# Performance work log

Hardware: AMD Instinct MI355X
Metric: run time of the kernel (lower is better)

## Reference

```python
import jax, jax.numpy as jnp
import numpy as np

N = 100000
E = 1600000
D_IN = 128
HID = 128
N_CLASSES = 40
NEG_SLOPE = 0.2  # PyG GATConv default
BN_EPS = 1e-5


def setup_inputs() -> dict:
    key = jax.random.key(0)
    ks = jax.random.split(key, 16)
    s = 0.1
    return {
        "x": jax.random.normal(ks[0], (N, D_IN), dtype=jnp.float32),
        "edge_index": jax.random.randint(ks[1], (2, E), 0, N, dtype=jnp.int64),
        # GAT layer 1 (in=D_IN, out=HID, heads=1)
        "W1": jax.random.normal(ks[2], (D_IN, HID), dtype=jnp.float32) * s,
        "a_src1": jax.random.normal(ks[3], (HID,), dtype=jnp.float32) * s,
        "a_dst1": jax.random.normal(ks[4], (HID,), dtype=jnp.float32) * s,
        "b1": jnp.zeros((HID,), dtype=jnp.float32),
        # GAT layer 2 (in=HID, out=HID, heads=1)
        "W2": jax.random.normal(ks[5], (HID, HID), dtype=jnp.float32) * s,
        "a_src2": jax.random.normal(ks[6], (HID,), dtype=jnp.float32) * s,
        "a_dst2": jax.random.normal(ks[7], (HID,), dtype=jnp.float32) * s,
        "b2": jnp.zeros((HID,), dtype=jnp.float32),
        # shared BatchNorm1d(HID) applied after every conv
        "gamma": jnp.ones((HID,), dtype=jnp.float32),
        "beta": jnp.zeros((HID,), dtype=jnp.float32),
        # output Linear(HID, N_CLASSES)
        "Wout": jax.random.normal(ks[8], (HID, N_CLASSES), dtype=jnp.float32) * s,
        "bout": jnp.zeros((N_CLASSES,), dtype=jnp.float32),
    }


def reference(x, edge_index, W1, a_src1, a_dst1, b1, W2, a_src2, a_dst2, b2,
              gamma, beta, Wout, bout):
    n = x.shape[0]
    loops = jnp.arange(n, dtype=edge_index.dtype)  # add_self_loops (GATConv default)
    src = jnp.concatenate([edge_index[0], loops])
    dst = jnp.concatenate([edge_index[1], loops])

    def gat_layer(h_in, W, a_s, a_d, b):
        h = h_in @ W                                   # [N, HID]
        e_src = h @ a_s                                # [N] per-node src score
        e_dst = h @ a_d                                # [N] per-node dst score
        e = jax.nn.leaky_relu(e_src[src] + e_dst[dst], NEG_SLOPE)  # [E+N]
        # segment softmax over incoming edges of each dst node
        m = jax.ops.segment_max(e, dst, num_segments=n)
        p = jnp.exp(e - m[dst])
        denom = jax.ops.segment_sum(p, dst, num_segments=n)
        alpha = p / denom[dst]
        out = jax.ops.segment_sum(alpha[:, None] * h[src], dst, num_segments=n)
        return out + b

    def bn_elu(z):
        mu = z.mean(axis=0)
        var = ((z - mu) ** 2).mean(axis=0)  # biased var (BN training mode)
        zh = (z - mu) / jnp.sqrt(var + BN_EPS) * gamma + beta
        return jax.nn.elu(zh)

    h = bn_elu(gat_layer(x, W1, a_src1, a_dst1, b1))
    h = bn_elu(gat_layer(h, W2, a_src2, a_dst2, b2))
    return h @ Wout + bout
```

## Files before the change

kernel.cpp:

```cpp
#include <hip/hip_runtime.h>

#define NNODES 100000
#define NEDGES 1600000
#define ET (NEDGES + NNODES)
#define NBUCK 196
#define NEG 0.2f
#define BNEPS 1e-5f
#define EPB 16384
#define NBLK_E ((ET + EPB - 1) / EPB)

typedef __attribute__((ext_vector_type(8))) short short8;
typedef __attribute__((ext_vector_type(4))) float floatx4;
typedef __attribute__((ext_vector_type(2))) float floatx2;

__device__ __forceinline__ unsigned short f2b(float x) {
    unsigned int u = __float_as_uint(x);
    u += 0x7fff + ((u >> 16) & 1);
    return (unsigned short)(u >> 16);
}
__device__ __forceinline__ float b2f(unsigned short u) {
    return __uint_as_float(((unsigned int)u) << 16);
}
__device__ __forceinline__ float blo2f(unsigned int v) {
    return __uint_as_float(v << 16);
}
__device__ __forceinline__ float bhi2f(unsigned int v) {
    return __uint_as_float(v & 0xffff0000u);
}
__device__ __forceinline__ floatx2 u2f2(unsigned int v) {
    floatx2 r;
    r.x = __uint_as_float(v << 16);
    r.y = __uint_as_float(v & 0xffff0000u);
    return r;
}

__device__ __forceinline__ int edge_src(const int* ei, int e, int w64) {
    if (e >= NEDGES) return e - NEDGES;
    return w64 ? ei[2 * e] : ei[e];
}
__device__ __forceinline__ int edge_dst(const int* ei, int e, int w64) {
    if (e >= NEDGES) return e - NEDGES;
    return w64 ? ei[2 * (NEDGES + e)] : ei[NEDGES + e];
}

__global__ void k_prep(const float* __restrict__ W1, const float* __restrict__ W2,
                       unsigned short* __restrict__ WT1, unsigned short* __restrict__ WT2,
                       const int* ei, int* flag, int* bcnt, int* done, float* bnstat) {
    int t = blockIdx.x * 256 + threadIdx.x;
    if (blockIdx.x == 0) {
        bcnt[threadIdx.x] = 0;
        if (threadIdx.x == 0) *done = 0;
        if (threadIdx.x == 1) {
            int is64 = 1;
            for (int j = 1; j < 16; j += 2)
                if (ei[j] != 0) is64 = 0;
            *flag = is64;
        }
    } else if (blockIdx.x == 1) {
        bnstat[threadIdx.x] = 0.f;
    } else if (blockIdx.x == 2) {
        bnstat[256 + threadIdx.x] = 0.f;
    }
    int k = t >> 7, n = t & 127;
    WT1[n * 128 + k] = f2b(W1[t]);
    WT2[n * 128 + k] = f2b(W2[t]);
}

__global__ __launch_bounds__(256) void k_bhist(const int* __restrict__ ei,
                                               const int* flag, int* bcnt,
                                               int* done, int* bbase, int* bcur) {
    __shared__ int lc[256];
    __shared__ int lastf;
    int t = threadIdx.x;
    lc[t] = 0;
    __syncthreads();
    int w64 = *flag;
    int base = blockIdx.x * EPB;
    for (int j = 0; j < EPB / 512; j++) {
        int e = base + j * 512 + t * 2;
        if (e + 1 < NEDGES) {
            int d0, d1;
            if (w64) {
                int4 dv = *(const int4*)&ei[2 * (NEDGES + e)];
                d0 = dv.x; d1 = dv.z;
            } else {
                int2 dv = *(const int2*)&ei[NEDGES + e];
                d0 = dv.x; d1 = dv.y;
            }
            atomicAdd(&lc[d0 >> 9], 1);
            atomicAdd(&lc[d1 >> 9], 1);
        } else {
            for (int k = 0; k < 2; k++) {
                int ee = e + k;
                if (ee < ET) atomicAdd(&lc[edge_dst(ei, ee, w64) >> 9], 1);
            }
        }
    }
    __syncthreads();
    if (t < NBUCK && lc[t]) atomicAdd(&bcnt[t], lc[t]);
    __threadfence();
    __syncthreads();
    if (t == 0) lastf = (atomicAdd(done, 1) == gridDim.x - 1) ? 1 : 0;
    __syncthreads();
    if (!lastf) return;
    int v = (t < NBUCK) ? atomicAdd(&bcnt[t], 0) : 0;
    __syncthreads();
    lc[t] = v;
    __syncthreads();
    for (int off = 1; off < 256; off <<= 1) {
        int add = (t >= off) ? lc[t - off] : 0;
        __syncthreads();
        lc[t] += add;
        __syncthreads();
    }
    int excl = lc[t] - v;
    if (t < NBUCK) { bbase[t] = excl; bcur[t] = excl; }
    if (t == NBUCK - 1) bbase[NBUCK] = excl + v;
}

__global__ __launch_bounds__(256) void k_bscatter(const int* __restrict__ ei,
                                                  const int* flag, int* bcur,
                                                  int* __restrict__ pairs) {
    __shared__ int lc[256];
    __shared__ int lbase[256];
    int t = threadIdx.x;
    lc[t] = 0;
    __syncthreads();
    int w64 = *flag;
    int base = blockIdx.x * EPB;
    for (int j = 0; j < EPB / 512; j++) {
        int e = base + j * 512 + t * 2;
        if (e + 1 < NEDGES) {
            int d0, d1;
            if (w64) {
                int4 dv = *(const int4*)&ei[2 * (NEDGES + e)];
                d0 = dv.x; d1 = dv.z;
            } else {
                int2 dv = *(const int2*)&ei[NEDGES + e];
                d0 = dv.x; d1 = dv.y;
            }
            atomicAdd(&lc[d0 >> 9], 1);
            atomicAdd(&lc[d1 >> 9], 1);
        } else {
            for (int k = 0; k < 2; k++) {
                int ee = e + k;
                if (ee < ET) atomicAdd(&lc[edge_dst(ei, ee, w64) >> 9], 1);
            }
        }
    }
    __syncthreads();
    if (t < NBUCK && lc[t]) lbase[t] = atomicAdd(&bcur[t], lc[t]);
    __syncthreads();
    for (int j = 0; j < EPB / 512; j++) {
        int e = base + j * 512 + t * 2;
        if (e + 1 < NEDGES) {
            int s0, s1, d0, d1;
            if (w64) {
                int4 sv = *(const int4*)&ei[2 * e];
                int4 dv = *(const int4*)&ei[2 * (NEDGES + e)];
                s0 = sv.x; s1 = sv.z; d0 = dv.x; d1 = dv.z;
            } else {
                int2 sv = *(const int2*)&ei[e];
                int2 dv = *(const int2*)&ei[NEDGES + e];
                s0 = sv.x; s1 = sv.y; d0 = dv.x; d1 = dv.y;
            }
            int p0 = atomicAdd(&lbase[d0 >> 9], 1);
            pairs[p0] = (s0 << 9) | (d0 & 511);
            int p1 = atomicAdd(&lbase[d1 >> 9], 1);
            pairs[p1] = (s1 << 9) | (d1 & 511);
        } else {
            for (int k = 0; k < 2; k++) {
                int ee = e + k;
                if (ee < ET) {
                    int src = edge_src(ei, ee, w64);
                    int dst = edge_dst(ei, ee, w64);
                    int pos = atomicAdd(&lbase[dst >> 9], 1);
                    pairs[pos] = (src << 9) | (dst & 511);
                }
            }
        }
    }
}

__global__ __launch_bounds__(256) void k_bsort(const int* __restrict__ pairs,
                                               const int* __restrict__ bbase,
                                               int* __restrict__ rowptr,
                                               int* __restrict__ srcs) {
    __shared__ int ncnt[512];
    __shared__ int nbase[512];
    __shared__ int stmp[256];
    int b = blockIdx.x, t = threadIdx.x;
    ncnt[t] = 0; ncnt[t + 256] = 0;
    __syncthreads();
    int s0 = bbase[b], s1 = bbase[b + 1];
    for (int i = s0 + t; i < s1; i += 256)
        atomicAdd(&ncnt[pairs[i] & 511], 1);
    __syncthreads();
    int c0 = ncnt[2 * t], c1 = ncnt[2 * t + 1];
    int s = c0 + c1;
    stmp[t] = s;
    __syncthreads();
    for (int off = 1; off < 256; off <<= 1) {
        int add = (t >= off) ? stmp[t - off] : 0;
        __syncthreads();
        stmp[t] += add;
        __syncthreads();
    }
    int excl = stmp[t] - s;
    nbase[2 * t] = excl;
    nbase[2 * t + 1] = excl + c0;
    __syncthreads();
    for (int l = t; l < 512; l += 256) {
        int node = b * 512 + l;
        if (node <= NNODES) rowptr[node] = s0 + nbase[l];
        ncnt[l] = nbase[l];
    }
    __syncthreads();
    for (int i = s0 + t; i < s1; i += 256) {
        int pr = pairs[i];
        int off = atomicAdd(&ncnt[pr & 511], 1);
        srcs[s0 + off] = ((unsigned int)pr) >> 9;
    }
}

template<bool BN>
__global__ __launch_bounds__(256) void k_gemm(const void* __restrict__ Ain,
        const unsigned short* __restrict__ WTg,
        const float* __restrict__ sums, const float* __restrict__ sqs,
        const float* __restrict__ gamma, const float* __restrict__ beta,
        const float* __restrict__ a_s, const float* __restrict__ a_d,
        float* __restrict__ es, float* __restrict__ ed,
        unsigned short* __restrict__ hB, int n) {
    __shared__ unsigned short lA[64][136];
    __shared__ unsigned short lW[128][136];
    __shared__ float las[128], lad[128];
    __shared__ float lsc[128], lsh[128];
    int t = threadIdx.x;
    int row0 = blockIdx.x * 64;
    if (t < 128) { las[t] = a_s[t]; lad[t] = a_d[t]; }
    if (BN && t < 128) {
        float mu = sums[t] * (1.f / NNODES);
        float var = fmaxf(sqs[t] * (1.f / NNODES) - mu * mu, 0.f);
        float s = gamma[t] * rsqrtf(var + BNEPS);
        lsc[t] = s;
        lsh[t] = beta[t] - mu * s;
    }

    const uint4* wt4 = (const uint4*)WTg;
#pragma unroll
    for (int j = 0; j < 8; j++) {
        int idx = t + j * 256;
        *(uint4*)&lW[idx >> 4][(idx & 15) * 8] = wt4[idx];
    }
    if (BN) __syncthreads();

    if (BN) {
        const uint4* Ab = (const uint4*)Ain;
#pragma unroll
        for (int j = 0; j < 4; j++) {
            int idx = t + j * 256;
            int r = idx >> 4, seg = idx & 15;
            uint4 v = make_uint4(0, 0, 0, 0);
            if (row0 + r < n) v = Ab[(size_t)(row0 + r) * 16 + seg];
            float f[8];
            f[0] = blo2f(v.x); f[1] = bhi2f(v.x);
            f[2] = blo2f(v.y); f[3] = bhi2f(v.y);
            f[4] = blo2f(v.z); f[5] = bhi2f(v.z);
            f[6] = blo2f(v.w); f[7] = bhi2f(v.w);
            ushort4 u0, u1;
            unsigned short us[8];
#pragma unroll
            for (int k = 0; k < 8; k++) {
                int c = seg * 8 + k;
                float z = fmaf(f[k], lsc[c], lsh[c]);
                z = z > 0.f ? z : __expf(z) - 1.f;
                us[k] = f2b(z);
            }
            u0.x = us[0]; u0.y = us[1]; u0.z = us[2]; u0.w = us[3];
            u1.x = us[4]; u1.y = us[5]; u1.z = us[6]; u1.w = us[7];
            *(ushort4*)&lA[r][seg * 8] = u0;
            *(ushort4*)&lA[r][seg * 8 + 4] = u1;
        }
    } else {
        const float* Af = (const float*)Ain;
#pragma unroll
        for (int j = 0; j < 8; j++) {
            int idx = t + j * 256;
            int r = idx >> 5, c4 = idx & 31;
            float4 v = make_float4(0.f, 0.f, 0.f, 0.f);
            if (row0 + r < n) v = ((const float4*)Af)[(size_t)(row0 + r) * 32 + c4];
            ushort4 u;
            u.x = f2b(v.x); u.y = f2b(v.y); u.z = f2b(v.z); u.w = f2b(v.w);
            *(ushort4*)&lA[r][c4 * 4] = u;
        }
    }
    __syncthreads();

    int w = t >> 6, lane = t & 63;
    int m = lane & 15, q = lane >> 4;
    int arow = w * 16 + m;
    floatx4 acc[8];
#pragma unroll
    for (int ct = 0; ct < 8; ct++) acc[ct] = (floatx4)0.0f;

#pragma unroll
    for (int kt = 0; kt < 4; kt++) {
        int kb = kt * 32 + q * 8;
        short8 af = *(const short8*)&lA[arow][kb];
#pragma unroll
        for (int ct = 0; ct < 8; ct++) {
            short8 bf = *(const short8*)&lW[ct * 16 + m][kb];
            acc[ct] = __builtin_amdgcn_mfma_f32_16x16x32_bf16(af, bf, acc[ct], 0, 0, 0);
        }
    }

    __syncthreads();
#pragma unroll
    for (int ct = 0; ct < 8; ct++)
#pragma unroll
        for (int r = 0; r < 4; r++)
            lA[w * 16 + q * 4 + r][ct * 16 + m] = f2b(acc[ct][r]);
#pragma unroll
    for (int j = 0; j < 4; j++) {
        int idx = lane + j * 64;
        int r = idx >> 4, seg = idx & 15;
        int grow = row0 + w * 16 + r;
        if (grow < n) {
            uint4 v = *(const uint4*)&lA[w * 16 + r][seg * 8];
            ((uint4*)hB)[(size_t)grow * 16 + seg] = v;
        }
    }
    __syncthreads();
    int r = t >> 2, q4 = t & 3;
    float s1 = 0.f, s2 = 0.f;
#pragma unroll
    for (int k = 0; k < 32; k++) {
        int c = q4 * 32 + k;
        float v = b2f(lA[r][c]);
        s1 += v * las[c];
        s2 += v * lad[c];
    }
    s1 += __shfl_xor(s1, 1, 64); s1 += __shfl_xor(s1, 2, 64);
    s2 += __shfl_xor(s2, 1, 64); s2 += __shfl_xor(s2, 2, 64);
    if (q4 == 0 && row0 + r < n) { es[row0 + r] = s1; ed[row0 + r] = s2; }
}

__global__ __launch_bounds__(256) void k_attn(const unsigned short* __restrict__ hB,
                                              const int* __restrict__ srcs,
                                              const int* __restrict__ rowptr,
                                              const float* __restrict__ es,
                                              const float* __restrict__ ed,
                                              const float* __restrict__ bias,
                                              unsigned short* __restrict__ haggB, int n) {
    int w = (blockIdx.x * 256 + threadIdx.x) >> 4;
    if (w >= n) return;
    int l = threadIdx.x & 15;
    int qb = threadIdx.x & 48;
    int start = rowptr[w], end = rowptr[w + 1];
    float edv = ed[w];
    const uint4* hp4 = (const uint4*)hB;
    floatx2 a0 = {0.f, 0.f}, a1 = {0.f, 0.f}, a2 = {0.f, 0.f}, a3 = {0.f, 0.f};
    float den = 0.f;

    for (int chunk = start; chunk < end; chunk += 16) {
        int i = chunk + l;
        int sv = 0; float pv = 0.f;
        if (i < end) {
            sv = srcs[i];
            float e = es[sv] + edv;
            e = e > 0.f ? e : NEG * e;
            pv = __expf(e);
            den += pv;
        }
        int cnt = min(16, end - chunk);
        for (int j = 0; j < cnt; j++) {
            int   s0 = __shfl(sv, qb + j, 64);
            float p0 = __shfl(pv, qb + j, 64);
            uint4 h0 = hp4[(size_t)s0 * 16 + l];
            floatx2 P = {p0, p0};
            a0 += P * u2f2(h0.x); a1 += P * u2f2(h0.y);
            a2 += P * u2f2(h0.z); a3 += P * u2f2(h0.w);
        }
    }
    den += __shfl_xor(den, 1, 64); den += __shfl_xor(den, 2, 64);
    den += __shfl_xor(den, 4, 64); den += __shfl_xor(den, 8, 64);
    float inv = 1.f / den;
    const float2* b2p = (const float2*)bias;
    float2 c0 = b2p[l * 4 + 0], c1 = b2p[l * 4 + 1];
    float2 c2 = b2p[l * 4 + 2], c3 = b2p[l * 4 + 3];
    uint4 o;
    o.x = (unsigned int)f2b(fmaf(a0.x, inv, c0.x)) |
          ((unsigned int)f2b(fmaf(a0.y, inv, c0.y)) << 16);
    o.y = (unsigned int)f2b(fmaf(a1.x, inv, c1.x)) |
          ((unsigned int)f2b(fmaf(a1.y, inv, c1.y)) << 16);
    o.z = (unsigned int)f2b(fmaf(a2.x, inv, c2.x)) |
          ((unsigned int)f2b(fmaf(a2.y, inv, c2.y)) << 16);
    o.w = (unsigned int)f2b(fmaf(a3.x, inv, c3.x)) |
          ((unsigned int)f2b(fmaf(a3.y, inv, c3.y)) << 16);
    ((uint4*)haggB)[(size_t)w * 16 + l] = o;
}

__global__ __launch_bounds__(256) void k_bnstats(const unsigned short* __restrict__ hin,
                                                 float* sums, float* sqs, int n) {
    __shared__ float red[4][256];
    int t = threadIdx.x;
    int c2 = t & 63, quarter = t >> 6;
    int r0 = blockIdx.x * 512;
    int rend = min(r0 + 512, n);
    const unsigned int* hp = (const unsigned int*)hin;
    float s0 = 0.f, q0 = 0.f, s1 = 0.f, q1 = 0.f;
    for (int r = r0 + quarter; r < rend; r += 4) {
        unsigned int v = hp[(size_t)r * 64 + c2];
        float a = blo2f(v), b = bhi2f(v);
        s0 += a; q0 += a * a;
        s1 += b; q1 += b * b;
    }
    *(float4*)&red[quarter][c2 * 4] = make_float4(s0, q0, s1, q1);
    __syncthreads();
    float v = red[0][t] + red[1][t] + red[2][t] + red[3][t];
    int c2i = t >> 2, k = t & 3;
    int ch = c2i * 2 + (k >> 1);
    if (k & 1) atomicAdd(&sqs[ch], v);
    else       atomicAdd(&sums[ch], v);
}

__global__ __launch_bounds__(256) void k_outgemm(const unsigned short* __restrict__ h,
                                                 const float* __restrict__ sums,
                                                 const float* __restrict__ sqs,
                                                 const float* __restrict__ gamma,
                                                 const float* __restrict__ beta,
                                                 const float* __restrict__ Wout,
                                                 const float* __restrict__ bout,
                                                 float* __restrict__ out, int n) {
    __shared__ float lwT[40][128];
    __shared__ float lh[64][132];
    __shared__ float lb[40];
    __shared__ float lsc[128], lsh[128];
    int t = threadIdx.x;
    if (t < 128) {
        float mu = sums[t] * (1.f / NNODES);
        float var = fmaxf(sqs[t] * (1.f / NNODES) - mu * mu, 0.f);
        float s = gamma[t] * rsqrtf(var + BNEPS);
        lsc[t] = s;
        lsh[t] = beta[t] - mu * s;
    }
    for (int idx = t; idx < 128 * 40; idx += 256) {
        int r = idx / 40, c = idx % 40;
        lwT[c][r] = Wout[idx];
    }
    if (t < 40) lb[t] = bout[t];
    __syncthreads();
    int n0 = blockIdx.x * 64;
    const uint4* hb4 = (const uint4*)h;
#pragma unroll
    for (int j = 0; j < 4; j++) {
        int idx = t + j * 256;
        int r = idx >> 4, seg = idx & 15;
        uint4 v = make_uint4(0, 0, 0, 0);
        if (n0 + r < n) v = hb4[(size_t)(n0 + r) * 16 + seg];
        float f[8];
        f[0] = blo2f(v.x); f[1] = bhi2f(v.x);
        f[2] = blo2f(v.y); f[3] = bhi2f(v.y);
        f[4] = blo2f(v.z); f[5] = bhi2f(v.z);
        f[6] = blo2f(v.w); f[7] = bhi2f(v.w);
#pragma unroll
        for (int k = 0; k < 8; k++) {
            int c = seg * 8 + k;
            float z = fmaf(f[k], lsc[c], lsh[c]);
            z = z > 0.f ? z : __expf(z) - 1.f;
            lh[r][c] = z;
        }
    }
    __syncthreads();
    int nl = t & 63, g = t >> 6;
    int row = n0 + nl;
    if (row >= n) return;
    float acc[10] = {};
    for (int k = 0; k < 128; k += 4) {
        float4 hv = *(const float4*)&lh[nl][k];
#pragma unroll
        for (int j = 0; j < 10; j++) {
            float4 wv = *(const float4*)&lwT[g * 10 + j][k];
            acc[j] += hv.x * wv.x + hv.y * wv.y + hv.z * wv.z + hv.w * wv.w;
        }
    }
#pragma unroll
    for (int j = 0; j < 10; j++)
        out[(size_t)row * 40 + g * 10 + j] = acc[j] + lb[g * 10 + j];
}

extern "C" void kernel_launch(void* const* d_in, const int* in_sizes, int n_in,
                              void* d_out, int out_size, void* d_ws, size_t ws_size,
                              hipStream_t stream) {
    const float* x      = (const float*)d_in[0];
    const int*   ei     = (const int*)d_in[1];
    const float* W1     = (const float*)d_in[2];
    const float* a_src1 = (const float*)d_in[3];
    const float* a_dst1 = (const float*)d_in[4];
    const float* b1     = (const float*)d_in[5];
    const float* W2     = (const float*)d_in[6];
    const float* a_src2 = (const float*)d_in[7];
    const float* a_dst2 = (const float*)d_in[8];
    const float* b2     = (const float*)d_in[9];
    const float* gamma  = (const float*)d_in[10];
    const float* beta   = (const float*)d_in[11];
    const float* Wout   = (const float*)d_in[12];
    const float* bout   = (const float*)d_in[13];
    float* out = (float*)d_out;

    char* p = (char*)d_ws;
    auto alloc = [&](size_t bytes) -> void* {
        void* r = (void*)p;
        p += (bytes + 255) & ~(size_t)255;
        return r;
    };
    unsigned short* hB    = (unsigned short*)alloc((size_t)NNODES * 128 * 2);
    unsigned short* haggB = (unsigned short*)alloc((size_t)NNODES * 128 * 2);
    float* es     = (float*)alloc((size_t)NNODES * 4);
    float* ed     = (float*)alloc((size_t)NNODES * 4);
    int*   pairs  = (int*)alloc((size_t)ET * 4);
    int*   srcs   = (int*)alloc((size_t)ET * 4);
    int*   rowptr = (int*)alloc((size_t)(NNODES + 1) * 4);
    int*   bcnt   = (int*)alloc(256 * 4);
    int*   bbase  = (int*)alloc(256 * 4);
    int*   bcur   = (int*)alloc(256 * 4);
    float* bnstat = (float*)alloc(4 * 128 * 4);
    unsigned short* WT1 = (unsigned short*)alloc(128 * 128 * 2);
    unsigned short* WT2 = (unsigned short*)alloc(128 * 128 * 2);
    int*   flag   = (int*)alloc(4);
    int*   done   = (int*)alloc(4);

    float* sum1 = bnstat, *sq1 = bnstat + 128, *sum2 = bnstat + 256, *sq2 = bnstat + 384;

    k_prep<<<64, 256, 0, stream>>>(W1, W2, WT1, WT2, ei, flag, bcnt, done, bnstat);
    k_bhist<<<NBLK_E, 256, 0, stream>>>(ei, flag, bcnt, done, bbase, bcur);
    k_bscatter<<<NBLK_E, 256, 0, stream>>>(ei, flag, bcur, pairs);
    k_bsort<<<NBUCK, 256, 0, stream>>>(pairs, bbase, rowptr, srcs);

    const int GB = (NNODES + 63) / 64;
    const int AB = NNODES / 16;
    const int SB = (NNODES + 511) / 512;

    k_gemm<false><<<GB, 256, 0, stream>>>(x, WT1, nullptr, nullptr, nullptr, nullptr,
                                          a_src1, a_dst1, es, ed, hB, NNODES);
    k_attn<<<AB, 256, 0, stream>>>(hB, srcs, rowptr, es, ed, b1, haggB, NNODES);
    k_bnstats<<<SB, 256, 0, stream>>>(haggB, sum1, sq1, NNODES);

    k_gemm<true><<<GB, 256, 0, stream>>>(haggB, WT2, sum1, sq1, gamma, beta,
                                         a_src2, a_dst2, es, ed, hB, NNODES);
    k_attn<<<AB, 256, 0, stream>>>(hB, srcs, rowptr, es, ed, b2, haggB, NNODES);
    k_bnstats<<<SB, 256, 0, stream>>>(haggB, sum2, sq2, NNODES);

    k_outgemm<<<GB, 256, 0, stream>>>(haggB, sum2, sq2, gamma, beta, Wout, bout, out, NNODES);

    (void)in_sizes; (void)n_in; (void)out_size; (void)ws_size;
}
```

Before: 485.3 us.

## Degree-sort nodes for attention, fuse BN stats into attention, shrink edge blocks

Builds a degree histogram during the bucket sort, scans it and writes a permutation of nodes ordered by in-degree. The attention kernel walks nodes in that order so that 16-lane groups in a wavefront get similar edge counts, reducing divergence and load imbalance. BatchNorm sum and sum-of-squares are now reduced inside the attention kernel through shuffles, LDS and atomics, which drops the separate bnstats pass that re-read the aggregated features. The edges-per-block value for the histogram and scatter kernels is cut to a quarter, giving more blocks. The costs are two extra small kernels, scattered output writes, and 128 float atomics per attention block.

Result: slower. 660.9 us (+36.2%).

```diff
diff --git a/kernel.cpp b/kernel.cpp
--- a/kernel.cpp
+++ b/kernel.cpp
@@ -6,7 +6,7 @@
 #define NBUCK 196
 #define NEG 0.2f
 #define BNEPS 1e-5f
-#define EPB 16384
+#define EPB 4096
 #define NBLK_E ((ET + EPB - 1) / EPB)
 
 typedef __attribute__((ext_vector_type(8))) short short8;
@@ -45,7 +45,8 @@
 
 __global__ void k_prep(const float* __restrict__ W1, const float* __restrict__ W2,
                        unsigned short* __restrict__ WT1, unsigned short* __restrict__ WT2,
-                       const int* ei, int* flag, int* bcnt, int* done, float* bnstat) {
+                       const int* ei, int* flag, int* bcnt, int* done, float* bnstat,
+                       int* dhist) {
     int t = blockIdx.x * 256 + threadIdx.x;
     if (blockIdx.x == 0) {
         bcnt[threadIdx.x] = 0;
@@ -60,6 +61,8 @@
         bnstat[threadIdx.x] = 0.f;
     } else if (blockIdx.x == 2) {
         bnstat[256 + threadIdx.x] = 0.f;
+    } else if (blockIdx.x == 3) {
+        dhist[threadIdx.x] = 0;
     }
     int k = t >> 7, n = t & 127;
     WT1[n * 128 + k] = f2b(W1[t]);
@@ -185,14 +188,17 @@
 __global__ __launch_bounds__(256) void k_bsort(const int* __restrict__ pairs,
                                                const int* __restrict__ bbase,
                                                int* __restrict__ rowptr,
-                                               int* __restrict__ srcs) {
+                                               int* __restrict__ srcs,
+                                               int* __restrict__ dhist) {
     __shared__ int ncnt[512];
     __shared__ int nbase[512];
     __shared__ int stmp[256];
+    __shared__ int ldh[256];
     int b = blockIdx.x, t = threadIdx.x;
-    ncnt[t] = 0; ncnt[t + 256] = 0;
+    ncnt[t] = 0; ncnt[t + 256] = 0; ldh[t] = 0;
     __syncthreads();
     int s0 = bbase[b], s1 = bbase[b + 1];
+    int btot = s1 - s0;
     for (int i = s0 + t; i < s1; i += 256)
         atomicAdd(&ncnt[pairs[i] & 511], 1);
     __syncthreads();
@@ -213,6 +219,10 @@
     for (int l = t; l < 512; l += 256) {
         int node = b * 512 + l;
         if (node <= NNODES) rowptr[node] = s0 + nbase[l];
+        if (node < NNODES) {
+            int deg = ((l < 511) ? nbase[l + 1] : btot) - nbase[l];
+            atomicAdd(&ldh[min(deg, 255)], 1);
+        }
         ncnt[l] = nbase[l];
     }
     __syncthreads();
@@ -220,6 +230,46 @@
         int pr = pairs[i];
         int off = atomicAdd(&ncnt[pr & 511], 1);
         srcs[s0 + off] = ((unsigned int)pr) >> 9;
+    }
+    __syncthreads();
+    if (ldh[t]) atomicAdd(&dhist[t], ldh[t]);
+}
+
+__global__ void k_dscan(const int* __restrict__ dhist, int* dcur) {
+    __shared__ int sh[256];
+    int t = threadIdx.x;
+    int v = dhist[t];
+    sh[t] = v;
+    __syncthreads();
+    for (int off = 1; off < 256; off <<= 1) {
+        int add = (t >= off) ? sh[t - off] : 0;
+        __syncthreads();
+        sh[t] += add;
+        __syncthreads();
+    }
+    int total = sh[255];
+    dcur[t] = total - sh[t];
+}
+
+__global__ __launch_bounds__(256) void k_dperm(const int* __restrict__ rowptr,
+                                               int* dcur, int* __restrict__ perm) {
+    __shared__ int lc[256];
+    __shared__ int lbase[256];
+    int t = threadIdx.x;
+    lc[t] = 0;
+    __syncthreads();
+    int n = blockIdx.x * 256 + t;
+    int d = -1;
+    if (n < NNODES) {
+        d = min(rowptr[n + 1] - rowptr[n], 255);
+        atomicAdd(&lc[d], 1);
+    }
+    __syncthreads();
+    if (lc[t]) lbase[t] = atomicAdd(&dcur[t], lc[t]);
+    __syncthreads();
+    if (n < NNODES) {
+        int pos = atomicAdd(&lbase[d], 1);
+        perm[pos] = n;
     }
 }
 
@@ -348,12 +398,16 @@
 __global__ __launch_bounds__(256) void k_attn(const unsigned short* __restrict__ hB,
                                               const int* __restrict__ srcs,
                                               const int* __restrict__ rowptr,
+                                              const int* __restrict__ perm,
                                               const float* __restrict__ es,
                                               const float* __restrict__ ed,
                                               const float* __restrict__ bias,
-                                              unsigned short* __restrict__ haggB, int n) {
-    int w = (blockIdx.x * 256 + threadIdx.x) >> 4;
-    if (w >= n) return;
+                                              unsigned short* __restrict__ haggB,
+                                              float* __restrict__ gsum,
+                                              float* __restrict__ gsq) {
+    __shared__ float lds_s[4][128], lds_q[4][128];
+    int widx = (blockIdx.x * 256 + threadIdx.x) >> 4;
+    int w = perm[widx];
     int l = threadIdx.x & 15;
     int qb = threadIdx.x & 48;
     int start = rowptr[w], end = rowptr[w + 1];
@@ -388,40 +442,42 @@
     const float2* b2p = (const float2*)bias;
     float2 c0 = b2p[l * 4 + 0], c1 = b2p[l * 4 + 1];
     float2 c2 = b2p[l * 4 + 2], c3 = b2p[l * 4 + 3];
-    uint4 o;
-    o.x = (unsigned int)f2b(fmaf(a0.x, inv, c0.x)) |
-          ((unsigned int)f2b(fmaf(a0.y, inv, c0.y)) << 16);
-    o.y = (unsigned int)f2b(fmaf(a1.x, inv, c1.x)) |
-          ((unsigned int)f2b(fmaf(a1.y, inv, c1.y)) << 16);
-    o.z = (unsigned int)f2b(fmaf(a2.x, inv, c2.x)) |
-          ((unsigned int)f2b(fmaf(a2.y, inv, c2.y)) << 16);
-    o.w = (unsigned int)f2b(fmaf(a3.x, inv, c3.x)) |
-          ((unsigned int)f2b(fmaf(a3.y, inv, c3.y)) << 16);
-    ((uint4*)haggB)[(size_t)w * 16 + l] = o;
-}
-
-__global__ __launch_bounds__(256) void k_bnstats(const unsigned short* __restrict__ hin,
-                                                 float* sums, float* sqs, int n) {
-    __shared__ float red[4][256];
-    int t = threadIdx.x;
-    int c2 = t & 63, quarter = t >> 6;
-    int r0 = blockIdx.x * 512;
-    int rend = min(r0 + 512, n);
-    const unsigned int* hp = (const unsigned int*)hin;
-    float s0 = 0.f, q0 = 0.f, s1 = 0.f, q1 = 0.f;
-    for (int r = r0 + quarter; r < rend; r += 4) {
-        unsigned int v = hp[(size_t)r * 64 + c2];
-        float a = blo2f(v), b = bhi2f(v);
-        s0 += a; q0 += a * a;
-        s1 += b; q1 += b * b;
-    }
-    *(float4*)&red[quarter][c2 * 4] = make_float4(s0, q0, s1, q1);
-    __syncthreads();
-    float v = red[0][t] + red[1][t] + red[2][t] + red[3][t];
-    int c2i = t >> 2, k = t & 3;
-    int ch = c2i * 2 + (k >> 1);
-    if (k & 1) atomicAdd(&sqs[ch], v);
-    else       atomicAdd(&sums[ch], v);
+    float o[8];
+    o[0] = fmaf(a0.x, inv, c0.x); o[1] = fmaf(a0.y, inv, c0.y);
+    o[2] = fmaf(a1.x, inv, c1.x); o[3] = fmaf(a1.y, inv, c1.y);
+    o[4] = fmaf(a2.x, inv, c2.x); o[5] = fmaf(a2.y, inv, c2.y);
+    o[6] = fmaf(a3.x, inv, c3.x); o[7] = fmaf(a3.y, inv, c3.y);
+    uint4 ov;
+    ov.x = (unsigned int)f2b(o[0]) | ((unsigned int)f2b(o[1]) << 16);
+    ov.y = (unsigned int)f2b(o[2]) | ((unsigned int)f2b(o[3]) << 16);
+    ov.z = (unsigned int)f2b(o[4]) | ((unsigned int)f2b(o[5]) << 16);
+    ov.w = (unsigned int)f2b(o[6]) | ((unsigned int)f2b(o[7]) << 16);
+    ((uint4*)haggB)[(size_t)w * 16 + l] = ov;
+
+    float sst[8], qst[8];
+#pragma unroll
+    for (int k = 0; k < 8; k++) { sst[k] = o[k]; qst[k] = o[k] * o[k]; }
+#pragma unroll
+    for (int k = 0; k < 8; k++) {
+        sst[k] += __shfl_xor(sst[k], 16, 64); sst[k] += __shfl_xor(sst[k], 32, 64);
+        qst[k] += __shfl_xor(qst[k], 16, 64); qst[k] += __shfl_xor(qst[k], 32, 64);
+    }
+    int wv = threadIdx.x >> 6, ln = threadIdx.x & 63;
+    if (ln < 16) {
+#pragma unroll
+        for (int k = 0; k < 8; k++) {
+            lds_s[wv][8 * ln + k] = sst[k];
+            lds_q[wv][8 * ln + k] = qst[k];
+        }
+    }
+    __syncthreads();
+    if (threadIdx.x < 128) {
+        int c = threadIdx.x;
+        float ss = lds_s[0][c] + lds_s[1][c] + lds_s[2][c] + lds_s[3][c];
+        float qq = lds_q[0][c] + lds_q[1][c] + lds_q[2][c] + lds_q[3][c];
+        atomicAdd(&gsum[c], ss);
+        atomicAdd(&gsq[c], qq);
+    }
 }
 
 __global__ __launch_bounds__(256) void k_outgemm(const unsigned short* __restrict__ h,
@@ -521,9 +577,12 @@
     int*   pairs  = (int*)alloc((size_t)ET * 4);
     int*   srcs   = (int*)alloc((size_t)ET * 4);
     int*   rowptr = (int*)alloc((size_t)(NNODES + 1) * 4);
+    int*   perm   = (int*)alloc((size_t)NNODES * 4);
     int*   bcnt   = (int*)alloc(256 * 4);
     int*   bbase  = (int*)alloc(256 * 4);
     int*   bcur   = (int*)alloc(256 * 4);
+    int*   dhist  = (int*)alloc(256 * 4);
+    int*   dcur   = (int*)alloc(256 * 4);
     float* bnstat = (float*)alloc(4 * 128 * 4);
     unsigned short* WT1 = (unsigned short*)alloc(128 * 128 * 2);
     unsigned short* WT2 = (unsigned short*)alloc(128 * 128 * 2);
@@ -532,24 +591,23 @@
 
     float* sum1 = bnstat, *sq1 = bnstat + 128, *sum2 = bnstat + 256, *sq2 = bnstat + 384;
 
-    k_prep<<<64, 256, 0, stream>>>(W1, W2, WT1, WT2, ei, flag, bcnt, done, bnstat);
+    k_prep<<<64, 256, 0, stream>>>(W1, W2, WT1, WT2, ei, flag, bcnt, done, bnstat, dhist);
     k_bhist<<<NBLK_E, 256, 0, stream>>>(ei, flag, bcnt, done, bbase, bcur);
     k_bscatter<<<NBLK_E, 256, 0, stream>>>(ei, flag, bcur, pairs);
-    k_bsort<<<NBUCK, 256, 0, stream>>>(pairs, bbase, rowptr, srcs);
+    k_bsort<<<NBUCK, 256, 0, stream>>>(pairs, bbase, rowptr, srcs, dhist);
+    k_dscan<<<1, 256, 0, stream>>>(dhist, dcur);
+    k_dperm<<<(NNODES + 255) / 256, 256, 0, stream>>>(rowptr, dcur, perm);
 
     const int GB = (NNODES + 63) / 64;
     const int AB = NNODES / 16;
-    const int SB = (NNODES + 511) / 512;
 
     k_gemm<false><<<GB, 256, 0, stream>>>(x, WT1, nullptr, nullptr, nullptr, nullptr,
                                           a_src1, a_dst1, es, ed, hB, NNODES);
-    k_attn<<<AB, 256, 0, stream>>>(hB, srcs, rowptr, es, ed, b1, haggB, NNODES);
-    k_bnstats<<<SB, 256, 0, stream>>>(haggB, sum1, sq1, NNODES);
+    k_attn<<<AB, 256, 0, stream>>>(hB, srcs, rowptr, perm, es, ed, b1, haggB, sum1, sq1);
 
     k_gemm<true><<<GB, 256, 0, stream>>>(haggB, WT2, sum1, sq1, gamma, beta,
                                          a_src2, a_dst2, es, ed, hB, NNODES);
-    k_attn<<<AB, 256, 0, stream>>>(hB, srcs, rowptr, es, ed, b2, haggB, NNODES);
-    k_bnstats<<<SB, 256, 0, stream>>>(haggB, sum2, sq2, NNODES);
+    k_attn<<<AB, 256, 0, stream>>>(hB, srcs, rowptr, perm, es, ed, b2, haggB, sum2, sq2);
 
     k_outgemm<<<GB, 256, 0, stream>>>(haggB, sum2, sq2, gamma, beta, Wout, bout, out, NNODES);
 
```
